# Optimization experiments

Hardware: AMD Instinct MI355X
Metric: run time of the kernel (lower is better)

Reference implementation:

```python
import jax, jax.numpy as jnp
import numpy as np

BS, H, L, D = 16, 16, 4096, 32  # bs, n_heads, seq_len(=q_len), head_dim

def setup_inputs() -> dict:
    key = jax.random.key(0)
    kq, kk, kv = jax.random.split(key, 3)
    q = jax.random.normal(kq, (BS, H, L, D), dtype=jnp.float32)
    k = jax.random.normal(kk, (BS, H, D, L), dtype=jnp.float32)
    v = jax.random.normal(kv, (BS, H, L, D), dtype=jnp.float32)
    return {"q": q, "k": k, "v": v}

def reference(q, k, v):
    # reordered attention: scores = (k @ v) / sqrt(seq_len) -> [bs,h,d_k,d_v]
    seq_len = v.shape[2]
    scores = jnp.einsum('bhds,bhse->bhde', k, v) / jnp.sqrt(jnp.float32(seq_len))
    # faithful to source: softmax over dim=0 (the batch dimension)
    attn_weights = jax.nn.softmax(scores, axis=0)
    # dropout p=0.0 -> identity
    # output = q @ weights -> [bs,h,q_len,d_v]
    output = jnp.einsum('bhld,bhde->bhle', q, attn_weights)
    return output, attn_weights
```

## Files before the change

kernel.cpp:

```cpp
#include <hip/hip_runtime.h>

#define BS 16
#define NH 16
#define LQ 4096
#define DH 32

constexpr size_t OUT_ELEMS = (size_t)BS * NH * LQ * DH;
constexpr int HDE = NH * DH * DH;

__device__ __forceinline__ void fma4(float4& a, float s, const float4& v) {
    a.x = fmaf(s, v.x, a.x);
    a.y = fmaf(s, v.y, a.y);
    a.z = fmaf(s, v.z, a.z);
    a.w = fmaf(s, v.w, a.w);
}

template<int NCH>
__global__ __launch_bounds__(256, 2) void kv_partial(const float* __restrict__ k,
                                                     const float* __restrict__ v,
                                                     float* __restrict__ part) {
    __shared__ float lds[8192];
    const int tid = threadIdx.x;
    const int w   = tid >> 6;
    const int l   = tid & 63;
    const int nsplit = 32 / NCH;
    const int p  = blockIdx.x % nsplit;
    const int bh = blockIdx.x / nsplit;

    const int tw = tid & 31;
    const int sp = tid >> 5;
    const int dg = tw >> 3;
    const int eg = tw & 7;
    const int d0 = dg << 3;
    const int e0 = eg << 2;

    const float* kb = k + (size_t)bh * DH * LQ;
    const float* vb = v + (size_t)bh * LQ * DH;
    float* kt = lds;
    float* vt = lds + 4096;

    const int kr   = tid >> 3;
    const int km   = tid & 7;
    const int kswz = (kr >> 2) & 7;
    const int vs   = tid >> 1;
    const int vh   = tid & 1;
    const int vswz = vs & 7;

    float4 acc[8];
#pragma unroll
    for (int i = 0; i < 8; ++i) acc[i] = make_float4(0.f, 0.f, 0.f, 0.f);

#pragma unroll
    for (int c = 0; c < NCH; ++c) {
        const int s0 = (p * NCH + c) << 7;
        if (c > 0) __syncthreads();

        float4 kst[4], vst[4];
#pragma unroll
        for (int j = 0; j < 4; ++j)
            kst[j] = *(const float4*)(kb + (size_t)kr * LQ + s0 + ((km + 8 * j) << 2));
#pragma unroll
        for (int j = 0; j < 4; ++j)
            vst[j] = *(const float4*)(vb + ((size_t)(s0 + vs) << 5) + (vh << 4) + (j << 2));
#pragma unroll
        for (int j = 0; j < 4; ++j)
            *(float4*)(kt + (kr << 7) + (((km + 8 * j) ^ kswz) << 2)) = kst[j];
#pragma unroll
        for (int j = 0; j < 4; ++j) {
            const int g = (vh << 2) + j;
            *(float4*)(vt + (vs << 5) + ((g ^ vswz) << 2)) = vst[j];
        }
        __syncthreads();

#pragma unroll
        for (int st = 0; st < 4; ++st) {
            const int cc = (sp << 2) + st;
            float4 kq[8];
#pragma unroll
            for (int i = 0; i < 8; ++i) {
                const int r = d0 + i;
                kq[i] = *(const float4*)(kt + (r << 7) + ((cc ^ ((r >> 2) & 7)) << 2));
            }
#pragma unroll
            for (int u = 0; u < 4; ++u) {
                const int s = (cc << 2) + u;
                const float4 vu = *(const float4*)(vt + (s << 5) + ((eg ^ (s & 7)) << 2));
#pragma unroll
                for (int i = 0; i < 8; ++i) {
                    const float ks = (u == 0) ? kq[i].x
                                   : (u == 1) ? kq[i].y
                                   : (u == 2) ? kq[i].z : kq[i].w;
                    fma4(acc[i], ks, vu);
                }
            }
        }
    }

#pragma unroll
    for (int i = 0; i < 8; ++i) {
        acc[i].x += __shfl_xor(acc[i].x, 32);
        acc[i].y += __shfl_xor(acc[i].y, 32);
        acc[i].z += __shfl_xor(acc[i].z, 32);
        acc[i].w += __shfl_xor(acc[i].w, 32);
    }

    __syncthreads();
    if (l < 32) {
        float* dst = lds + w * 1152 + l * 36;
#pragma unroll
        for (int i = 0; i < 8; ++i) *(float4*)(dst + (i << 2)) = acc[i];
    }
    __syncthreads();

    const int fdg = (tid >> 6) & 3;
    const int fi  = (tid >> 3) & 7;
    const int feg = tid & 7;
    const int off = (fdg * 8 + feg) * 36 + (fi << 2);
    float4 r0 = *(const float4*)(lds + off);
    const float4 r1 = *(const float4*)(lds + 1152 + off);
    const float4 r2 = *(const float4*)(lds + 2304 + off);
    const float4 r3 = *(const float4*)(lds + 3456 + off);
    r0.x = (r0.x + r1.x) + (r2.x + r3.x);
    r0.y = (r0.y + r1.y) + (r2.y + r3.y);
    r0.z = (r0.z + r1.z) + (r2.z + r3.z);
    r0.w = (r0.w + r1.w) + (r2.w + r3.w);
    *(float4*)(part + ((size_t)p * (BS * NH) + bh) * 1024 + (tid << 2)) = r0;
}

__global__ __launch_bounds__(256) void reduce_p(const float* __restrict__ part,
                                                float* __restrict__ wts, int nsp) {
    const int gidx = blockIdx.x * 256 + threadIdx.x;
    float s = 0.f;
#pragma unroll 8
    for (int pp = 0; pp < nsp; ++pp)
        s += part[((size_t)pp << 18) + gidx];
    wts[gidx] = s * (1.0f / 64.0f);
}

__global__ __launch_bounds__(256) void softmax_b(float* __restrict__ wts) {
    const int idx = blockIdx.x * 256 + threadIdx.x;

    float sc[BS];
#pragma unroll
    for (int b = 0; b < BS; ++b) sc[b] = wts[((size_t)b << 14) + idx];
    float m = sc[0];
#pragma unroll
    for (int b = 1; b < BS; ++b) m = fmaxf(m, sc[b]);
    float sum = 0.f;
#pragma unroll
    for (int b = 0; b < BS; ++b) { sc[b] = __expf(sc[b] - m); sum += sc[b]; }
    const float inv = 1.0f / sum;
#pragma unroll
    for (int b = 0; b < BS; ++b) wts[((size_t)b << 14) + idx] = sc[b] * inv;
}

__global__ __launch_bounds__(256, 2) void qw(const float* __restrict__ q,
                                             const float* __restrict__ wts,
                                             float* __restrict__ out) {
    __shared__ float qs[128 * 36];
    const int blk = blockIdx.x;
    const int bh  = blk >> 5;
    const int lt  = blk & 31;
    const int tid = threadIdx.x;

    const float* qbase = q + ((size_t)bh * LQ + lt * 128) * DH;

#pragma unroll
    for (int pp = 0; pp < 4; ++pp) {
        const int idx = pp * 256 + tid;
        const int row = idx >> 3;
        const int c4  = idx & 7;
        const float4 t = *(const float4*)(qbase + idx * 4);
        *(float4*)(qs + row * 36 + c4 * 4) = t;
    }

    const int lsub = tid >> 3;
    const int e0   = (tid & 7) << 2;

    const int b = bh >> 4, h = bh & 15;
    float4 Wf[32];
    const float* wbase = wts + ((size_t)b << 14) + ((size_t)h << 10) + e0;
#pragma unroll
    for (int d = 0; d < 32; ++d) Wf[d] = *(const float4*)(wbase + d * DH);

    __syncthreads();

    float* obase = out + ((size_t)bh * LQ + lt * 128) * DH;

#pragma unroll
    for (int r = 0; r < 4; ++r) {
        const int lr = lsub + r * 32;
        const float* qrow = qs + lr * 36;
        float4 acc = {0, 0, 0, 0};
#pragma unroll
        for (int d4 = 0; d4 < 32; d4 += 4) {
            const float4 qv = *(const float4*)(qrow + d4);
            fma4(acc, qv.x, Wf[d4 + 0]);
            fma4(acc, qv.y, Wf[d4 + 1]);
            fma4(acc, qv.z, Wf[d4 + 2]);
            fma4(acc, qv.w, Wf[d4 + 3]);
        }
        *(float4*)(obase + (size_t)lr * DH + e0) = acc;
    }
}

extern "C" void kernel_launch(void* const* d_in, const int* in_sizes, int n_in,
                              void* d_out, int out_size, void* d_ws, size_t ws_size,
                              hipStream_t stream) {
    const float* q = (const float*)d_in[0];
    const float* k = (const float*)d_in[1];
    const float* v = (const float*)d_in[2];
    float* out  = (float*)d_out;
    float* wts  = out + OUT_ELEMS;
    float* part = (float*)d_ws;

    const size_t need32 = (size_t)32 * 256 * 1024 * 4;
    int nsp;
    if (ws_size >= need32) {
        kv_partial<1><<<256 * 32, 256, 0, stream>>>(k, v, part);
        nsp = 32;
    } else {
        kv_partial<4><<<256 * 8, 256, 0, stream>>>(k, v, part);
        nsp = 8;
    }
    reduce_p<<<(BS * HDE) / 256, 256, 0, stream>>>(part, wts, nsp);
    softmax_b<<<HDE / 256, 256, 0, stream>>>(wts);
    qw<<<BS * NH * (LQ / 128), 256, 0, stream>>>(q, wts, out);
}
```

Baseline: 134.8 us.

## Prefetch next K/V chunk into registers and fix split count to eight

The kv_partial kernel now loads the next 128-column chunk of K and V into registers while computing on the current chunk in LDS, then writes it to LDS after a barrier. This is register-level software pipelining meant to hide global load latency. The launcher also drops the 32-way split path (used when workspace is large) and always uses 8 splits with 4 chunks each. That cuts partial-sum traffic and reduce work but gives fewer blocks, and the extra prefetch registers may lower occupancy.

```diff
diff --git a/kernel.cpp b/kernel.cpp
--- a/kernel.cpp
+++ b/kernel.cpp
@@ -7,6 +7,8 @@
 
 constexpr size_t OUT_ELEMS = (size_t)BS * NH * LQ * DH;
 constexpr int HDE = NH * DH * DH;
+constexpr int NSPLIT = 8;
+constexpr int NCH = 4;
 
 __device__ __forceinline__ void fma4(float4& a, float s, const float4& v) {
     a.x = fmaf(s, v.x, a.x);
@@ -15,7 +17,7 @@
     a.w = fmaf(s, v.w, a.w);
 }
 
-template<int NCH>
+template<int NCHT>
 __global__ __launch_bounds__(256, 2) void kv_partial(const float* __restrict__ k,
                                                      const float* __restrict__ v,
                                                      float* __restrict__ part) {
@@ -23,7 +25,7 @@
     const int tid = threadIdx.x;
     const int w   = tid >> 6;
     const int l   = tid & 63;
-    const int nsplit = 32 / NCH;
+    const int nsplit = 32 / NCHT;
     const int p  = blockIdx.x % nsplit;
     const int bh = blockIdx.x / nsplit;
 
@@ -32,7 +34,6 @@
     const int dg = tw >> 3;
     const int eg = tw & 7;
     const int d0 = dg << 3;
-    const int e0 = eg << 2;
 
     const float* kb = k + (size_t)bh * DH * LQ;
     const float* vb = v + (size_t)bh * LQ * DH;
@@ -50,12 +51,10 @@
 #pragma unroll
     for (int i = 0; i < 8; ++i) acc[i] = make_float4(0.f, 0.f, 0.f, 0.f);
 
-#pragma unroll
-    for (int c = 0; c < NCH; ++c) {
-        const int s0 = (p * NCH + c) << 7;
-        if (c > 0) __syncthreads();
-
-        float4 kst[4], vst[4];
+    float4 kst[4], vst[4];
+
+    {
+        const int s0 = (p * NCHT) << 7;
 #pragma unroll
         for (int j = 0; j < 4; ++j)
             kst[j] = *(const float4*)(kb + (size_t)kr * LQ + s0 + ((km + 8 * j) << 2));
@@ -71,6 +70,19 @@
             *(float4*)(vt + (vs << 5) + ((g ^ vswz) << 2)) = vst[j];
         }
         __syncthreads();
+    }
+
+#pragma unroll
+    for (int c = 0; c < NCHT; ++c) {
+        if (c + 1 < NCHT) {
+            const int s1 = (p * NCHT + c + 1) << 7;
+#pragma unroll
+            for (int j = 0; j < 4; ++j)
+                kst[j] = *(const float4*)(kb + (size_t)kr * LQ + s1 + ((km + 8 * j) << 2));
+#pragma unroll
+            for (int j = 0; j < 4; ++j)
+                vst[j] = *(const float4*)(vb + ((size_t)(s1 + vs) << 5) + (vh << 4) + (j << 2));
+        }
 
 #pragma unroll
         for (int st = 0; st < 4; ++st) {
@@ -93,6 +105,19 @@
                     fma4(acc[i], ks, vu);
                 }
             }
+        }
+
+        if (c + 1 < NCHT) {
+            __syncthreads();
+#pragma unroll
+            for (int j = 0; j < 4; ++j)
+                *(float4*)(kt + (kr << 7) + (((km + 8 * j) ^ kswz) << 2)) = kst[j];
+#pragma unroll
+            for (int j = 0; j < 4; ++j) {
+                const int g = (vh << 2) + j;
+                *(float4*)(vt + (vs << 5) + ((g ^ vswz) << 2)) = vst[j];
+            }
+            __syncthreads();
         }
     }
 
@@ -214,16 +239,8 @@
     float* wts  = out + OUT_ELEMS;
     float* part = (float*)d_ws;
 
-    const size_t need32 = (size_t)32 * 256 * 1024 * 4;
-    int nsp;
-    if (ws_size >= need32) {
-        kv_partial<1><<<256 * 32, 256, 0, stream>>>(k, v, part);
-        nsp = 32;
-    } else {
-        kv_partial<4><<<256 * 8, 256, 0, stream>>>(k, v, part);
-        nsp = 8;
-    }
-    reduce_p<<<(BS * HDE) / 256, 256, 0, stream>>>(part, wts, nsp);
+    kv_partial<NCH><<<BS * NH * NSPLIT, 256, 0, stream>>>(k, v, part);
+    reduce_p<<<(BS * HDE) / 256, 256, 0, stream>>>(part, wts, NSPLIT);
     softmax_b<<<HDE / 256, 256, 0, stream>>>(wts);
     qw<<<BS * NH * (LQ / 128), 256, 0, stream>>>(q, wts, out);
 }
```

New measurement: 177.7 us. +31.9%, slower.
